# Optimization experiments

Hardware: AMD Instinct MI355X
Metric: run time of the kernel (lower is better)

Reference implementation:

```python
import jax, jax.numpy as jnp
import numpy as np

B, L, E, D = 32, 1024, 512, 512  # batch, seq_len, input_size, per-direction hidden
SCALE = 1.4142135623730951  # rescale=True, highway_bias=0 -> sqrt(1+exp(0*2)) = sqrt(2)


def setup_inputs() -> dict:
    key = jax.random.key(0)
    ks = jax.random.split(key, 12)
    g = lambda k, shape, s: (jax.random.normal(k, shape, jnp.float32) * s)
    return {
        "seqs": jax.random.normal(ks[0], (B, L, E), jnp.float32),
        # layer 0: input E -> 2 dirs * 4 projections * D
        "W0": g(ks[1], (E, 8 * D), (1.0 / E) ** 0.5),
        "vf0": g(ks[2], (2, D), 0.1), "vr0": g(ks[3], (2, D), 0.1),
        "bf0": jnp.zeros((2, D), jnp.float32), "br0": jnp.zeros((2, D), jnp.float32),
        # layer 1: input 2D -> 2 dirs * 4 projections * D
        "W1": g(ks[4], (2 * D, 8 * D), (1.0 / (2 * D)) ** 0.5),
        "vf1": g(ks[5], (2, D), 0.1), "vr1": g(ks[6], (2, D), 0.1),
        "bf1": jnp.zeros((2, D), jnp.float32), "br1": jnp.zeros((2, D), jnp.float32),
        "lengths": jax.random.randint(ks[7], (B,), 1, L + 1, dtype=jnp.int32),
    }


def _sru_dir(u, vf, vr, bf, br, reverse):
    # u: (L, B, 4, D) -> h: (L, B, D), c_T: (B, D)
    def step(c, u_t):
        xt, fp, rp, xp = u_t[:, 0], u_t[:, 1], u_t[:, 2], u_t[:, 3]
        f = jax.nn.sigmoid(fp + vf * c + bf)
        c_new = f * c + (1.0 - f) * xt
        r = jax.nn.sigmoid(rp + vr * c + br)
        h = r * c_new + (1.0 - r) * xp * SCALE
        return c_new, h

    c0 = jnp.zeros((u.shape[1], u.shape[-1]), u.dtype)
    cT, hs = jax.lax.scan(step, c0, u, reverse=reverse)
    return hs, cT


def _sru_layer(x, W, vf, vr, bf, br):
    # x: (L, B, n_in)
    Lx, Bx = x.shape[0], x.shape[1]
    U = (x @ W).reshape(Lx, Bx, 2, 4, -1)  # dirs, (x_tilde, f, r, x_resid)
    h_f, c_f = _sru_dir(U[:, :, 0], vf[0], vr[0], bf[0], br[0], False)
    h_b, c_b = _sru_dir(U[:, :, 1], vf[1], vr[1], bf[1], br[1], True)
    return jnp.concatenate([h_f, h_b], -1), jnp.concatenate([c_f, c_b], -1)


def reference(seqs, W0, vf0, vr0, bf0, br0, W1, vf1, vr1, bf1, br1, lengths):
    x = jnp.transpose(seqs, (1, 0, 2))  # (L, B, E)
    out0, _ = _sru_layer(x, W0, vf0, vr0, bf0, br0)
    out1, c1 = _sru_layer(out0, W1, vf1, vr1, bf1, br1)
    # module returns (h[1], output.transpose(0,1)): layer-1 final cell state, (B,L,2D) outputs
    return c1, jnp.transpose(out1, (1, 0, 2))
```

## Files before the change

### kernel.cpp

```cpp
#include <hip/hip_runtime.h>
#include <cstdint>
#include <cstddef>

#define B_   32
#define L_   1024
#define D_   512
#define M_   (B_ * L_)
#define N8D  4096
#define SCALEF 1.4142135623730951f
#define LOG2E 1.4426950408889634f

typedef unsigned short u16;
typedef __bf16 bf16x8 __attribute__((ext_vector_type(8)));
typedef unsigned short u16x8 __attribute__((ext_vector_type(8)));
typedef unsigned short u16x4 __attribute__((ext_vector_type(4)));
typedef float f32x4 __attribute__((ext_vector_type(4)));

__device__ __forceinline__ float bf2f(u16 u) {
    union { unsigned int i; float f; } v; v.i = ((unsigned int)u) << 16; return v.f;
}
__device__ __forceinline__ u16 f2bf(float x) {
    union { float f; unsigned int i; } v; v.f = x;
    unsigned int r = (v.i + 0x7fffu + ((v.i >> 16) & 1u)) >> 16;
    return (u16)r;
}
__device__ __forceinline__ float sigmoid_fast(float z) {
    return __builtin_amdgcn_rcpf(1.0f + __builtin_amdgcn_exp2f(-LOG2E * z));
}

__device__ __forceinline__ void gl2lds16(const u16* g, u16* l) {
    __builtin_amdgcn_global_load_lds(
        (const __attribute__((address_space(1))) void*)g,
        (__attribute__((address_space(3))) void*)l, 16, 0, 0);
}

#define VMW(n) asm volatile("s_waitcnt vmcnt(" #n ")" ::: "memory")
#define LGK(n) asm volatile("s_waitcnt lgkmcnt(" #n ")" ::: "memory")
#define SB     __builtin_amdgcn_sched_barrier(0)

__global__ __launch_bounds__(256) void f32_to_bf16(const float* __restrict__ in,
                                                   u16* __restrict__ out) {
    size_t i = ((size_t)blockIdx.x * 256 + threadIdx.x) * 8;
    f32x4 v0 = *(const f32x4*)(in + i);
    f32x4 v1 = *(const f32x4*)(in + i + 4);
    u16x8 o;
#pragma unroll
    for (int q = 0; q < 4; ++q) { o[q] = f2bf(v0[q]); o[4 + q] = f2bf(v1[q]); }
    *(u16x8*)(out + i) = o;
}

__global__ __launch_bounds__(256) void transpose_w(const float* __restrict__ in,
                                                   u16* __restrict__ out,
                                                   int R, int C) {
    __shared__ u16 tile[32][33];
    int bx = blockIdx.x * 32;
    int by = blockIdx.y * 32;
    int tx = threadIdx.x & 31;
    int ty = threadIdx.x >> 5;
#pragma unroll
    for (int i = 0; i < 32; i += 8)
        tile[ty + i][tx] = f2bf(in[(size_t)(by + ty + i) * C + bx + tx]);
    __syncthreads();
#pragma unroll
    for (int i = 0; i < 32; i += 8) {
        int n = bx + ty + i;
        int p = (n >> 11) * 2048 + ((n & 511) << 2) + ((n >> 9) & 3);
        out[(size_t)p * R + by + tx] = tile[tx][ty + i];
    }
}

__global__ __launch_bounds__(512, 2) void gemm256(const u16* __restrict__ A,
                                                  const u16* __restrict__ BT,
                                                  u16* __restrict__ U, int K) {
    extern __shared__ __align__(16) u16 lds[];
    const int t    = threadIdx.x;
    const int lane = t & 63;
    const int wave = t >> 6;
    const int wm   = wave >> 2;
    const int wn   = wave & 3;
    const int qm   = lane & 15;
    const int quad = lane >> 4;

    const int nwg = gridDim.x;
    const int wg  = blockIdx.x;
    const int swz = (wg & 7) * (nwg >> 3) + (wg >> 3);
    const int bn  = (swz & 15) << 8;
    const int bm  = (swz >> 4) << 8;

    const int P0   = t * 16;
    const int L0   = P0 ^ ((P0 >> 3) & 0x30);
    const int srow = L0 >> 6;
    const int scol = (L0 & 63) >> 1;
    const u16* Ag = A  + (size_t)(bm + srow) * K + scol;
    const u16* Bg = BT + (size_t)(bn + srow) * K + scol;
    const size_t g128 = (size_t)128 * K;
    u16* ldst = lds + t * 8;

    const int fxor  = (quad * 16) ^ ((qm & 6) << 3);
    const int aBase = (wm * 128 + qm) * 64 + fxor;
    const int bBase = (wn * 64  + qm) * 64 + fxor;
    const char* ldsc = (const char*)lds;

    f32x4 acc[8][4];
#pragma unroll
    for (int i = 0; i < 8; ++i)
#pragma unroll
        for (int j = 0; j < 4; ++j) acc[i][j] = (f32x4)(0.0f);

#define RD16(p) (*(const bf16x8*)(p))

#define STGR(op, tile, ks, buf) do {                                         \
        const u16* g_ = ((op) ? Bg : Ag) + (size_t)(tile) * 64 + (ks) * 32;  \
        u16* l_ = ldst + (buf) * 32768 + (op) * 16384 + (ks) * 8192;         \
        gl2lds16(g_, l_);                                                    \
        gl2lds16(g_ + g128, l_ + 4096);                                      \
    } while (0)

#define G4(g, av) do {                                                       \
        _Pragma("unroll")                                                    \
        for (int nj = 0; nj < 4; ++nj)                                       \
            acc[g][nj] = __builtin_amdgcn_mfma_f32_16x16x32_bf16(            \
                av, bb[nj], acc[g][nj], 0, 0, 0);                            \
    } while (0)

#define PH(buf, ks, stile, dostage, vmn, dobar) do {                         \
        const char* As_ = ldsc + ((buf) * 32768 + (ks) * 8192) * 2;          \
        const char* Bs_ = ldsc + ((buf) * 32768 + 16384 + (ks) * 8192) * 2;  \
        bf16x8 bb[4], aa[8];                                                 \
        bb[0] = RD16(Bs_ + bBase);        SB;                                \
        bb[1] = RD16(Bs_ + bBase + 1024); SB;                                \
        bb[2] = RD16(Bs_ + bBase + 2048); SB;                                \
        bb[3] = RD16(Bs_ + bBase + 3072); SB;                                \
        aa[0] = RD16(As_ + aBase);        SB;                                \
        aa[1] = RD16(As_ + aBase + 1024); SB;                                \
        aa[2] = RD16(As_ + aBase + 2048); SB;                                \
        aa[3] = RD16(As_ + aBase + 3072); SB;                                \
        aa[4] = RD16(As_ + aBase + 4096); SB;                                \
        aa[5] = RD16(As_ + aBase + 5120); SB;                                \
        aa[6] = RD16(As_ + aBase + 6144); SB;                                \
        aa[7] = RD16(As_ + aBase + 7168); SB;                                \
        if (dostage) { STGR(0, stile, ks, (buf) ^ 1);                        \
                       STGR(1, stile, ks, (buf) ^ 1); }                      \
        __builtin_amdgcn_s_setprio(1);                                       \
        LGK(7); SB; G4(0, aa[0]); SB;                                        \
        LGK(6); SB; G4(1, aa[1]); SB;                                        \
        LGK(5); SB; G4(2, aa[2]); SB;                                        \
        LGK(4); SB; G4(3, aa[3]); SB;                                        \
        LGK(3); SB; G4(4, aa[4]); SB;                                        \
        LGK(2); SB; G4(5, aa[5]); SB;                                        \
        LGK(1); SB; G4(6, aa[6]); SB;                                        \
        LGK(0); SB; G4(7, aa[7]); SB;                                        \
        __builtin_amdgcn_s_setprio(0);                                       \
        if ((vmn) == 4) VMW(4); else if ((vmn) == 0) VMW(0);                 \
        if (dobar) { SB; __builtin_amdgcn_s_barrier(); SB; }                 \
    } while (0)

    const int nt = K >> 6;

    STGR(0, 0, 0, 0); STGR(1, 0, 0, 0); STGR(0, 0, 1, 0); STGR(1, 0, 1, 0);
    VMW(4);
    __builtin_amdgcn_s_barrier();

    for (int i = 0; i < (nt >> 1) - 1; ++i) {
        const int t2 = 2 * i;
        PH(0, 0, t2 + 1, 1, 4, 1);
        PH(0, 1, t2 + 1, 1, 4, 1);
        PH(1, 0, t2 + 2, 1, 4, 1);
        PH(1, 1, t2 + 2, 1, 4, 1);
    }
    PH(0, 0, nt - 1, 1, 4, 1);
    PH(0, 1, nt - 1, 1, 4, 1);
    PH(1, 0, 0, 0, 0, 1);
    PH(1, 1, 0, 0, -1, 0);

#undef PH
#undef G4
#undef STGR
#undef RD16

#pragma unroll
    for (int i8 = 0; i8 < 8; ++i8) {
        const int row0 = bm + wm * 128 + (i8 >> 2) * 64 + (i8 & 3) * 16 + quad * 4;
#pragma unroll
        for (int nj = 0; nj < 4; ++nj) {
            const int col = bn + wn * 64 + nj * 16 + qm;
#pragma unroll
            for (int r = 0; r < 4; ++r)
                U[(size_t)(row0 + r) * N8D + col] = f2bf(acc[i8][nj][r]);
        }
    }
}

template<bool OUT_F32>
__global__ __launch_bounds__(64) void sru_scan(const u16* __restrict__ U,
                                               const float* __restrict__ vf,
                                               const float* __restrict__ vr,
                                               const float* __restrict__ bfv,
                                               const float* __restrict__ brv,
                                               void* __restrict__ Hv,
                                               void* __restrict__ Cv) {
    constexpr int PF = 32;
    constexpr int NB = L_ / PF;

    int gid = blockIdx.x * blockDim.x + threadIdx.x;
    int d   = gid & (D_ - 1);
    int dir = (gid >> 9) & 1;
    int b   = gid >> 10;
    int ch  = dir * D_ + d;

    const float vf_v = vf[ch];
    const float vr_v = vr[ch];
    const float bf_v = bfv[ch];
    const float br_v = brv[ch];

    const ptrdiff_t ustep = dir ? -(ptrdiff_t)N8D : (ptrdiff_t)N8D;
    const ptrdiff_t hstep = dir ? -(ptrdiff_t)1024 : (ptrdiff_t)1024;
    const u16* p0 = U + (size_t)b * L_ * N8D + dir * 2048 + d * 4
                      + (dir ? (size_t)(L_ - 1) * N8D : 0);
    const size_t hstart = (size_t)b * L_ * 1024 + ch + (dir ? (size_t)(L_ - 1) * 1024 : 0);
    float* Hf = (float*)Hv + hstart;
    u16*   Hh = (u16*)Hv + hstart;

    float c = 0.0f;

    auto loadB = [&](u16x4 (&buf)[PF], int tb) {
        const u16* base = p0 + (ptrdiff_t)tb * PF * ustep;
#pragma unroll
        for (int i = 0; i < PF; ++i)
            buf[i] = *(const u16x4*)(base + (ptrdiff_t)i * ustep);
    };
    auto compStore = [&](u16x4 (&buf)[PF], int tb) {
        const ptrdiff_t hb = (ptrdiff_t)tb * PF * hstep;
#pragma unroll
        for (int i = 0; i < PF; ++i) {
            float xt = bf2f(buf[i][0]), fp = bf2f(buf[i][1]);
            float rp = bf2f(buf[i][2]), xp = bf2f(buf[i][3]);
            float f = sigmoid_fast(fp + vf_v * c + bf_v);
            float r = sigmoid_fast(rp + vr_v * c + br_v);
            c = f * (c - xt) + xt;
            float xs = xp * SCALEF;
            float h  = r * (c - xs) + xs;
            ptrdiff_t ho = hb + (ptrdiff_t)i * hstep;
            if (OUT_F32) Hf[ho] = h; else Hh[ho] = f2bf(h);
        }
    };

    u16x4 b0[PF], b1[PF];
    loadB(b0, 0);
    loadB(b1, 1);
    for (int t = 0; t < NB; t += 2) {
        compStore(b0, t);
        if (t + 2 < NB) loadB(b0, t + 2);
        compStore(b1, t + 1);
        if (t + 3 < NB) loadB(b1, t + 3);
    }

    if (OUT_F32) ((float*)Cv)[b * 1024 + ch] = c;
    else         ((u16*)Cv)[b * 1024 + ch]  = f2bf(c);
}

extern "C" void kernel_launch(void* const* d_in, const int* in_sizes, int n_in,
                              void* d_out, int out_size, void* d_ws, size_t ws_size,
                              hipStream_t stream) {
    (void)in_sizes; (void)n_in; (void)out_size; (void)ws_size;

    const float* seqs = (const float*)d_in[0];
    const float* W0   = (const float*)d_in[1];
    const float* vf0  = (const float*)d_in[2];
    const float* vr0  = (const float*)d_in[3];
    const float* bf0  = (const float*)d_in[4];
    const float* br0  = (const float*)d_in[5];
    const float* W1   = (const float*)d_in[6];
    const float* vf1  = (const float*)d_in[7];
    const float* vr1  = (const float*)d_in[8];
    const float* bf1  = (const float*)d_in[9];
    const float* br1  = (const float*)d_in[10];

    float* out = (float*)d_out;
    char* ws = (char*)d_ws;

    const size_t U_BYTES  = (size_t)M_ * N8D * 2;
    const size_t H_BYTES  = (size_t)M_ * 1024 * 2;
    const size_t W0T_B    = (size_t)4096 * 512 * 2;
    const size_t W1T_B    = (size_t)4096 * 1024 * 2;

    u16* U   = (u16*)(ws);
    u16* H0  = (u16*)(ws + U_BYTES);
    u16* S16 = H0;
    u16* W0T = (u16*)(ws + U_BYTES + H_BYTES);
    u16* W1T = (u16*)(ws + U_BYTES + H_BYTES + W0T_B);
    u16* Cd  = (u16*)(ws + U_BYTES + H_BYTES + W0T_B + W1T_B);

    f32_to_bf16<<<dim3(M_ * 512 / 8 / 256), 256, 0, stream>>>(seqs, S16);

    transpose_w<<<dim3(4096 / 32, 512 / 32), 256, 0, stream>>>(W0, W0T, 512, 4096);
    transpose_w<<<dim3(4096 / 32, 1024 / 32), 256, 0, stream>>>(W1, W1T, 1024, 4096);

    gemm256<<<dim3(2048), 512, 131072, stream>>>(S16, W0T, U, 512);
    sru_scan<false><<<dim3(512), 64, 0, stream>>>(U, vf0, vr0, bf0, br0, (void*)H0, (void*)Cd);

    gemm256<<<dim3(2048), 512, 131072, stream>>>(H0, W1T, U, 1024);
    sru_scan<true><<<dim3(512), 64, 0, stream>>>(U, vf1, vr1, bf1, br1,
                                                 (void*)(out + B_ * 1024), (void*)out);
}
```

Before: 818.6 us.

## Shrink GEMM tile to 128x256 with 4 waves and triple-buffered K=32 pipeline

Replaces the 256x256, 8-wave GEMM with a 128x256 tile run by 4 waves, each wave covering all 128 rows and 64 columns. The K loop now steps by 32 with a three-stage ring of LDS buffers (73.7 KB), so tile kt+2 is loaded while kt is computed. Each step waits on one barrier and one vmcnt. The aim is smaller LDS per block, more blocks, and deeper prefetch to hide global latency. The cost is less reuse of the A/B tiles per block and twice as many barriers along K.

Result: no change. 807.5 us (-1.4%).

```diff
diff --git a/kernel.cpp b/kernel.cpp
--- a/kernel.cpp
+++ b/kernel.cpp
@@ -69,15 +69,13 @@
     }
 }
 
-__global__ __launch_bounds__(512, 2) void gemm256(const u16* __restrict__ A,
+__global__ __launch_bounds__(256, 2) void gemm128(const u16* __restrict__ A,
                                                   const u16* __restrict__ BT,
                                                   u16* __restrict__ U, int K) {
     extern __shared__ __align__(16) u16 lds[];
     const int t    = threadIdx.x;
     const int lane = t & 63;
-    const int wave = t >> 6;
-    const int wm   = wave >> 2;
-    const int wn   = wave & 3;
+    const int wn   = t >> 6;
     const int qm   = lane & 15;
     const int quad = lane >> 4;
 
@@ -85,7 +83,7 @@
     const int wg  = blockIdx.x;
     const int swz = (wg & 7) * (nwg >> 3) + (wg >> 3);
     const int bn  = (swz & 15) << 8;
-    const int bm  = (swz >> 4) << 8;
+    const int bm  = (swz >> 4) << 7;
 
     const int P0   = t * 16;
     const int L0   = P0 ^ ((P0 >> 3) & 0x30);
@@ -93,12 +91,12 @@
     const int scol = (L0 & 63) >> 1;
     const u16* Ag = A  + (size_t)(bm + srow) * K + scol;
     const u16* Bg = BT + (size_t)(bn + srow) * K + scol;
-    const size_t g128 = (size_t)128 * K;
+    const size_t g64 = (size_t)64 * K;
     u16* ldst = lds + t * 8;
 
-    const int fxor  = (quad * 16) ^ ((qm & 6) << 3);
-    const int aBase = (wm * 128 + qm) * 64 + fxor;
-    const int bBase = (wn * 64  + qm) * 64 + fxor;
+    const int fxor = (quad * 16) ^ ((qm & 6) << 3);
+    const int aL   = qm * 64 + fxor;
+    const int bL   = (wn * 64 + qm) * 64 + fxor;
     const char* ldsc = (const char*)lds;
 
     f32x4 acc[8][4];
@@ -109,38 +107,43 @@
 
 #define RD16(p) (*(const bf16x8*)(p))
 
-#define STGR(op, tile, ks, buf) do {                                         \
-        const u16* g_ = ((op) ? Bg : Ag) + (size_t)(tile) * 64 + (ks) * 32;  \
-        u16* l_ = ldst + (buf) * 32768 + (op) * 16384 + (ks) * 8192;         \
-        gl2lds16(g_, l_);                                                    \
-        gl2lds16(g_ + g128, l_ + 4096);                                      \
+#define STG6(kt, bb) do {                                                    \
+        const u16* a_ = Ag + (size_t)(kt) * 32;                              \
+        const u16* b_ = Bg + (size_t)(kt) * 32;                              \
+        u16* la = ldst + (bb) / 2;                                           \
+        gl2lds16(a_,       la);                                              \
+        gl2lds16(a_ + g64, la + 2048);                                       \
+        u16* lb = ldst + (bb) / 2 + 4096;                                    \
+        gl2lds16(b_,           lb);                                          \
+        gl2lds16(b_ + g64,     lb + 2048);                                   \
+        gl2lds16(b_ + 2 * g64, lb + 4096);                                   \
+        gl2lds16(b_ + 3 * g64, lb + 6144);                                   \
     } while (0)
 
 #define G4(g, av) do {                                                       \
         _Pragma("unroll")                                                    \
         for (int nj = 0; nj < 4; ++nj)                                       \
             acc[g][nj] = __builtin_amdgcn_mfma_f32_16x16x32_bf16(            \
-                av, bb[nj], acc[g][nj], 0, 0, 0);                            \
+                av, bbf[nj], acc[g][nj], 0, 0, 0);                           \
     } while (0)
 
-#define PH(buf, ks, stile, dostage, vmn, dobar) do {                         \
-        const char* As_ = ldsc + ((buf) * 32768 + (ks) * 8192) * 2;          \
-        const char* Bs_ = ldsc + ((buf) * 32768 + 16384 + (ks) * 8192) * 2;  \
-        bf16x8 bb[4], aa[8];                                                 \
-        bb[0] = RD16(Bs_ + bBase);        SB;                                \
-        bb[1] = RD16(Bs_ + bBase + 1024); SB;                                \
-        bb[2] = RD16(Bs_ + bBase + 2048); SB;                                \
-        bb[3] = RD16(Bs_ + bBase + 3072); SB;                                \
-        aa[0] = RD16(As_ + aBase);        SB;                                \
-        aa[1] = RD16(As_ + aBase + 1024); SB;                                \
-        aa[2] = RD16(As_ + aBase + 2048); SB;                                \
-        aa[3] = RD16(As_ + aBase + 3072); SB;                                \
-        aa[4] = RD16(As_ + aBase + 4096); SB;                                \
-        aa[5] = RD16(As_ + aBase + 5120); SB;                                \
-        aa[6] = RD16(As_ + aBase + 6144); SB;                                \
-        aa[7] = RD16(As_ + aBase + 7168); SB;                                \
-        if (dostage) { STGR(0, stile, ks, (buf) ^ 1);                        \
-                       STGR(1, stile, ks, (buf) ^ 1); }                      \
+#define PH(bb, STAGE_STMT, VM_STMT) do {                                     \
+        const char* As_ = ldsc + (bb);                                       \
+        const char* Bs_ = ldsc + (bb) + 8192;                                \
+        bf16x8 bbf[4], aa[8];                                                \
+        bbf[0] = RD16(Bs_ + bL);        SB;                                  \
+        bbf[1] = RD16(Bs_ + bL + 1024); SB;                                  \
+        bbf[2] = RD16(Bs_ + bL + 2048); SB;                                  \
+        bbf[3] = RD16(Bs_ + bL + 3072); SB;                                  \
+        aa[0] = RD16(As_ + aL);        SB;                                   \
+        aa[1] = RD16(As_ + aL + 1024); SB;                                   \
+        aa[2] = RD16(As_ + aL + 2048); SB;                                   \
+        aa[3] = RD16(As_ + aL + 3072); SB;                                   \
+        aa[4] = RD16(As_ + aL + 4096); SB;                                   \
+        aa[5] = RD16(As_ + aL + 5120); SB;                                   \
+        aa[6] = RD16(As_ + aL + 6144); SB;                                   \
+        aa[7] = RD16(As_ + aL + 7168); SB;                                   \
+        STAGE_STMT;                                                          \
         __builtin_amdgcn_s_setprio(1);                                       \
         LGK(7); SB; G4(0, aa[0]); SB;                                        \
         LGK(6); SB; G4(1, aa[1]); SB;                                        \
@@ -151,36 +154,34 @@
         LGK(1); SB; G4(6, aa[6]); SB;                                        \
         LGK(0); SB; G4(7, aa[7]); SB;                                        \
         __builtin_amdgcn_s_setprio(0);                                       \
-        if ((vmn) == 4) VMW(4); else if ((vmn) == 0) VMW(0);                 \
-        if (dobar) { SB; __builtin_amdgcn_s_barrier(); SB; }                 \
+        VM_STMT;                                                             \
+        SB; __builtin_amdgcn_s_barrier(); SB;                                \
     } while (0)
 
-    const int nt = K >> 6;
-
-    STGR(0, 0, 0, 0); STGR(1, 0, 0, 0); STGR(0, 0, 1, 0); STGR(1, 0, 1, 0);
-    VMW(4);
+    const int nt = K >> 5;
+
+    STG6(0, 0); STG6(1, 24576);
+    VMW(6);
     __builtin_amdgcn_s_barrier();
 
-    for (int i = 0; i < (nt >> 1) - 1; ++i) {
-        const int t2 = 2 * i;
-        PH(0, 0, t2 + 1, 1, 4, 1);
-        PH(0, 1, t2 + 1, 1, 4, 1);
-        PH(1, 0, t2 + 2, 1, 4, 1);
-        PH(1, 1, t2 + 2, 1, 4, 1);
+    int bb = 0, bs = 49152;
+    for (int tt = 0; tt + 2 < nt; ++tt) {
+        PH(bb, STG6(tt + 2, bs), VMW(6));
+        bb += 24576; if (bb == 73728) bb = 0;
+        bs += 24576; if (bs == 73728) bs = 0;
     }
-    PH(0, 0, nt - 1, 1, 4, 1);
-    PH(0, 1, nt - 1, 1, 4, 1);
-    PH(1, 0, 0, 0, 0, 1);
-    PH(1, 1, 0, 0, -1, 0);
+    PH(bb, , VMW(0));
+    bb += 24576; if (bb == 73728) bb = 0;
+    PH(bb, , );
 
 #undef PH
 #undef G4
-#undef STGR
+#undef STG6
 #undef RD16
 
 #pragma unroll
     for (int i8 = 0; i8 < 8; ++i8) {
-        const int row0 = bm + wm * 128 + (i8 >> 2) * 64 + (i8 & 3) * 16 + quad * 4;
+        const int row0 = bm + i8 * 16 + quad * 4;
 #pragma unroll
         for (int nj = 0; nj < 4; ++nj) {
             const int col = bn + wn * 64 + nj * 16 + qm;
@@ -296,10 +297,10 @@
     transpose_w<<<dim3(4096 / 32, 512 / 32), 256, 0, stream>>>(W0, W0T, 512, 4096);
     transpose_w<<<dim3(4096 / 32, 1024 / 32), 256, 0, stream>>>(W1, W1T, 1024, 4096);
 
-    gemm256<<<dim3(2048), 512, 131072, stream>>>(S16, W0T, U, 512);
+    gemm128<<<dim3(4096), 256, 73728, stream>>>(S16, W0T, U, 512);
     sru_scan<false><<<dim3(512), 64, 0, stream>>>(U, vf0, vr0, bf0, br0, (void*)H0, (void*)Cd);
 
-    gemm256<<<dim3(2048), 512, 131072, stream>>>(H0, W1T, U, 1024);
+    gemm128<<<dim3(4096), 256, 73728, stream>>>(H0, W1T, U, 1024);
     sru_scan<true><<<dim3(512), 64, 0, stream>>>(U, vf1, vr1, bf1, br1,
                                                  (void*)(out + B_ * 1024), (void*)out);
 }
```
